# Kernel tuning notes

Hardware: AMD Instinct MI355X
Metric: run time of the kernel (lower is better)

## Reference

```python
import jax, jax.numpy as jnp
import numpy as np

B, S, V, D = 64, 1024, 1024, 512


def setup_inputs() -> dict:
    key = jax.random.key(0)
    ks = jax.random.split(key, 18)
    sd = 1.0 / np.sqrt(D)
    return dict(
        map_memory=jnp.zeros((B, S, V), jnp.float32),
        step_memory=jnp.zeros((B, S, S), jnp.float32),
        evidence=jax.random.normal(ks[0], (B, D), jnp.float32),
        marker_id=jax.random.randint(ks[1], (B,), 0, 4, jnp.int32),
        source_idx=jax.random.randint(ks[2], (B,), 0, S, jnp.int32),
        source_mask=jax.random.randint(ks[3], (B,), 0, 2, jnp.int32).astype(bool),
        target_symbol_idx=jax.random.randint(ks[4], (B,), 0, S, jnp.int32),
        target_symbol_mask=jax.random.randint(ks[5], (B,), 0, 2, jnp.int32).astype(bool),
        target_value_idx=jax.random.randint(ks[6], (B,), 0, V, jnp.int32),
        target_value_mask=jax.random.randint(ks[7], (B,), 0, 2, jnp.int32).astype(bool),
        map_W1=jax.random.normal(ks[8], (D, D), jnp.float32) * sd,
        map_b1=jnp.zeros((D,), jnp.float32),
        map_W2=jax.random.normal(ks[9], (D, 1), jnp.float32) * sd,
        map_b2=jnp.zeros((1,), jnp.float32),
        step_W1=jax.random.normal(ks[10], (D, D), jnp.float32) * sd,
        step_b1=jnp.zeros((D,), jnp.float32),
        step_W2=jax.random.normal(ks[11], (D, 1), jnp.float32) * sd,
        step_b2=jnp.zeros((1,), jnp.float32),
    )


def _gain(x, W1, b1, W2, b2):
    # Dense -> gelu (flax default: approximate) -> Dense(1)
    h = jax.nn.gelu(x @ W1 + b1)
    return (h @ W2 + b2)[:, 0]  # [B]


def reference(map_memory, step_memory, evidence, marker_id, source_idx,
              source_mask, target_symbol_idx, target_symbol_mask,
              target_value_idx, target_value_mask,
              map_W1, map_b1, map_W2, map_b2,
              step_W1, step_b1, step_W2, step_b2):
    map_gate = jax.nn.sigmoid(_gain(evidence, map_W1, map_b1, map_W2, map_b2))    # [B]
    step_gate = jax.nn.sigmoid(_gain(evidence, step_W1, step_b1, step_W2, step_b2))  # [B]
    map_mask = ((marker_id == 1) | (marker_id == 2)) & source_mask & target_value_mask
    step_mask = (marker_id == 3) & source_mask & target_symbol_mask
    b = jnp.arange(map_memory.shape[0])
    # one-hot outer product 'bs,bv->bsv' * gate is exactly a single gated entry at
    # (source_idx, target_idx) per batch element -> indexed scatter-add.
    next_map = map_memory.at[b, source_idx, target_value_idx].add(
        map_gate * map_mask.astype(map_gate.dtype))
    next_step = step_memory.at[b, source_idx, target_symbol_idx].add(
        step_gate * step_mask.astype(step_gate.dtype))
    return next_map, next_step
```

## Files before the change

kernel.cpp:

```cpp
#include <hip/hip_runtime.h>
#include <math.h>

#define BB 64
#define SS 1024
#define VV 1024
#define DD 512

#define MAP_WORDS  ((size_t)BB * SS * VV)
#define STEP_WORDS ((size_t)BB * SS * SS)
#define TOT_WORDS  (MAP_WORDS + STEP_WORDS)
#define TOT_F4     (TOT_WORDS / 4)
#define MAP_F4     (MAP_WORDS / 4)

#define COPY_BLOCKS   16384
#define F4_PER_BLOCK  2048
#define NGATES        (BB * 2)
#define TOTAL_BLOCKS  (COPY_BLOCKS + NGATES)

typedef float f32x4 __attribute__((ext_vector_type(4)));

__device__ __forceinline__ float gelu_tanh(float x) {
    const float k = 0.7978845608028654f;
    float x3 = x * x * x;
    return 0.5f * x * (1.0f + tanhf(k * (x + 0.044715f * x3)));
}

__global__ void __launch_bounds__(256)
fused_copy_gate_kernel(
    const f32x4* __restrict__ map_memory,
    const f32x4* __restrict__ step_memory,
    f32x4* __restrict__ out,
    const float* __restrict__ evidence,
    const int* __restrict__ marker_id,
    const int* __restrict__ source_idx,
    const int* __restrict__ source_mask,
    const int* __restrict__ target_symbol_idx,
    const int* __restrict__ target_symbol_mask,
    const int* __restrict__ target_value_idx,
    const int* __restrict__ target_value_mask,
    const float* __restrict__ map_W1, const float* __restrict__ map_b1,
    const float* __restrict__ map_W2, const float* __restrict__ map_b2,
    const float* __restrict__ step_W1, const float* __restrict__ step_b1,
    const float* __restrict__ step_W2, const float* __restrict__ step_b2,
    int* __restrict__ ws_idx, float* __restrict__ ws_g)
{
    const int blk = blockIdx.x;
    if (blk < COPY_BLOCKS) {
        const size_t base = (size_t)blk * F4_PER_BLOCK + threadIdx.x;
        const f32x4* __restrict__ src =
            (blk < COPY_BLOCKS / 2) ? (map_memory + base)
                                    : (step_memory + (base - MAP_F4));
        f32x4* __restrict__ dst = out + base;
        f32x4 v0 = src[0 * 256];
        f32x4 v1 = src[1 * 256];
        f32x4 v2 = src[2 * 256];
        f32x4 v3 = src[3 * 256];
        f32x4 v4 = src[4 * 256];
        f32x4 v5 = src[5 * 256];
        f32x4 v6 = src[6 * 256];
        f32x4 v7 = src[7 * 256];
        dst[0 * 256] = v0;
        dst[1 * 256] = v1;
        dst[2 * 256] = v2;
        dst[3 * 256] = v3;
        dst[4 * 256] = v4;
        dst[5 * 256] = v5;
        dst[6 * 256] = v6;
        dst[7 * 256] = v7;
        return;
    }

    const int gb   = blk - COPY_BLOCKS;
    const int b    = gb >> 1;
    const int head = gb & 1;
    const float* W1  = head ? step_W1 : map_W1;
    const float* b1  = head ? step_b1 : map_b1;
    const float* W2  = head ? step_W2 : map_W2;
    const float* b2v = head ? step_b2 : map_b2;

    __shared__ float ev[DD];
    __shared__ float wsum[4];

    const int tid = threadIdx.x;
    for (int i = tid; i < DD; i += 256) ev[i] = evidence[b * DD + i];
    __syncthreads();

    float acc = 0.0f;
    #pragma unroll
    for (int jj = 0; jj < DD; jj += 256) {
        const int j = jj + tid;
        float h = b1[j];
        #pragma unroll 8
        for (int k = 0; k < DD; ++k) {
            h = fmaf(ev[k], W1[k * DD + j], h);
        }
        h = gelu_tanh(h);
        acc = fmaf(h, W2[j], acc);
    }

    #pragma unroll
    for (int off = 32; off > 0; off >>= 1) acc += __shfl_down(acc, off, 64);
    if ((tid & 63) == 0) wsum[tid >> 6] = acc;
    __syncthreads();

    if (tid == 0) {
        float g = wsum[0] + wsum[1] + wsum[2] + wsum[3] + b2v[0];
        g = 1.0f / (1.0f + expf(-g));
        const int m  = marker_id[b];
        const bool sm = source_mask[b] != 0;
        int idx = -1;
        if (head == 0) {
            if (((m == 1) || (m == 2)) && sm && (target_value_mask[b] != 0)) {
                idx = b * (SS * VV) + source_idx[b] * VV + target_value_idx[b];
            }
        } else {
            if ((m == 3) && sm && (target_symbol_mask[b] != 0)) {
                idx = (int)MAP_WORDS + b * (SS * SS) + source_idx[b] * SS
                    + target_symbol_idx[b];
            }
        }
        ws_idx[gb] = idx;
        ws_g[gb]   = g;
    }
}

__global__ void __launch_bounds__(NGATES)
scatter_tail_kernel(const int* __restrict__ ws_idx,
                    const float* __restrict__ ws_g,
                    float* __restrict__ out)
{
    const int i = threadIdx.x;
    const int idx = ws_idx[i];
    if (idx >= 0) out[idx] += ws_g[i];
}

extern "C" void kernel_launch(void* const* d_in, const int* in_sizes, int n_in,
                              void* d_out, int out_size, void* d_ws, size_t ws_size,
                              hipStream_t stream) {
    const float* map_memory  = (const float*)d_in[0];
    const float* step_memory = (const float*)d_in[1];
    const float* evidence    = (const float*)d_in[2];
    const int* marker_id     = (const int*)d_in[3];
    const int* source_idx    = (const int*)d_in[4];
    const int* source_mask        = (const int*)d_in[5];
    const int* target_symbol_idx  = (const int*)d_in[6];
    const int* target_symbol_mask = (const int*)d_in[7];
    const int* target_value_idx   = (const int*)d_in[8];
    const int* target_value_mask  = (const int*)d_in[9];
    const float* map_W1  = (const float*)d_in[10];
    const float* map_b1  = (const float*)d_in[11];
    const float* map_W2  = (const float*)d_in[12];
    const float* map_b2  = (const float*)d_in[13];
    const float* step_W1 = (const float*)d_in[14];
    const float* step_b1 = (const float*)d_in[15];
    const float* step_W2 = (const float*)d_in[16];
    const float* step_b2 = (const float*)d_in[17];

    float* out = (float*)d_out;
    char* ws = (char*)d_ws;
    int*   ws_idx = (int*)ws;
    float* ws_g   = (float*)(ws + NGATES * sizeof(int));

    fused_copy_gate_kernel<<<dim3(TOTAL_BLOCKS), dim3(256), 0, stream>>>(
        (const f32x4*)map_memory, (const f32x4*)step_memory, (f32x4*)out,
        evidence, marker_id, source_idx, source_mask,
        target_symbol_idx, target_symbol_mask,
        target_value_idx, target_value_mask,
        map_W1, map_b1, map_W2, map_b2,
        step_W1, step_b1, step_W2, step_b2,
        ws_idx, ws_g);

    scatter_tail_kernel<<<dim3(1), dim3(NGATES), 0, stream>>>(ws_idx, ws_g, out);
}
```

Measured before the change: 256.8 us.

## Use grid-stride nontemporal copy and schedule gate blocks first

Replaces the 16384 fixed-size copy blocks with 4096 persistent grid-stride blocks that copy both memories using nontemporal loads and stores. The gate MLP blocks now take the lowest block indices, so they are dispatched first and overlap with the bandwidth-bound copy instead of trailing it. Nontemporal hints are meant to keep the streaming copy from polluting the caches, at the cost of less memory-level parallelism per thread than the previous eight-deep unrolled loads.

Result: faster. 236.8 us (-7.8%).

```diff
diff --git a/kernel.cpp b/kernel.cpp
--- a/kernel.cpp
+++ b/kernel.cpp
@@ -11,11 +11,11 @@
 #define TOT_WORDS  (MAP_WORDS + STEP_WORDS)
 #define TOT_F4     (TOT_WORDS / 4)
 #define MAP_F4     (MAP_WORDS / 4)
+#define STEP_F4    (STEP_WORDS / 4)
 
-#define COPY_BLOCKS   16384
-#define F4_PER_BLOCK  2048
-#define NGATES        (BB * 2)
-#define TOTAL_BLOCKS  (COPY_BLOCKS + NGATES)
+#define COPY_BLOCKS  4096
+#define NGATES       (BB * 2)
+#define TOTAL_BLOCKS (COPY_BLOCKS + NGATES)
 
 typedef float f32x4 __attribute__((ext_vector_type(4)));
 
@@ -26,7 +26,7 @@
 }
 
 __global__ void __launch_bounds__(256)
-fused_copy_gate_kernel(
+fused_gate_copy_kernel(
     const f32x4* __restrict__ map_memory,
     const f32x4* __restrict__ step_memory,
     f32x4* __restrict__ out,
@@ -44,33 +44,24 @@
     const float* __restrict__ step_W2, const float* __restrict__ step_b2,
     int* __restrict__ ws_idx, float* __restrict__ ws_g)
 {
-    const int blk = blockIdx.x;
-    if (blk < COPY_BLOCKS) {
-        const size_t base = (size_t)blk * F4_PER_BLOCK + threadIdx.x;
-        const f32x4* __restrict__ src =
-            (blk < COPY_BLOCKS / 2) ? (map_memory + base)
-                                    : (step_memory + (base - MAP_F4));
-        f32x4* __restrict__ dst = out + base;
-        f32x4 v0 = src[0 * 256];
-        f32x4 v1 = src[1 * 256];
-        f32x4 v2 = src[2 * 256];
-        f32x4 v3 = src[3 * 256];
-        f32x4 v4 = src[4 * 256];
-        f32x4 v5 = src[5 * 256];
-        f32x4 v6 = src[6 * 256];
-        f32x4 v7 = src[7 * 256];
-        dst[0 * 256] = v0;
-        dst[1 * 256] = v1;
-        dst[2 * 256] = v2;
-        dst[3 * 256] = v3;
-        dst[4 * 256] = v4;
-        dst[5 * 256] = v5;
-        dst[6 * 256] = v6;
-        dst[7 * 256] = v7;
+    if (blockIdx.x >= NGATES) {
+        const int cblk = blockIdx.x - NGATES;
+        const size_t stride = (size_t)COPY_BLOCKS * 256;
+        const size_t tid0 = (size_t)cblk * 256 + threadIdx.x;
+        #pragma unroll 4
+        for (size_t i = tid0; i < MAP_F4; i += stride) {
+            f32x4 v = __builtin_nontemporal_load(&map_memory[i]);
+            __builtin_nontemporal_store(v, &out[i]);
+        }
+        #pragma unroll 4
+        for (size_t i = tid0; i < STEP_F4; i += stride) {
+            f32x4 v = __builtin_nontemporal_load(&step_memory[i]);
+            __builtin_nontemporal_store(v, &out[MAP_F4 + i]);
+        }
         return;
     }
 
-    const int gb   = blk - COPY_BLOCKS;
+    const int gb   = blockIdx.x;
     const int b    = gb >> 1;
     const int head = gb & 1;
     const float* W1  = head ? step_W1 : map_W1;
@@ -161,7 +152,7 @@
     int*   ws_idx = (int*)ws;
     float* ws_g   = (float*)(ws + NGATES * sizeof(int));
 
-    fused_copy_gate_kernel<<<dim3(TOTAL_BLOCKS), dim3(256), 0, stream>>>(
+    fused_gate_copy_kernel<<<dim3(TOTAL_BLOCKS), dim3(256), 0, stream>>>(
         (const f32x4*)map_memory, (const f32x4*)step_memory, (f32x4*)out,
         evidence, marker_id, source_idx, source_mask,
         target_symbol_idx, target_symbol_mask,
```
